# Optimization experiments

Hardware: AMD Instinct MI355X
Metric: run time of the kernel (lower is better)

The kernel has to match this reference:

```python
import jax, jax.numpy as jnp
import numpy as np

B, N, D, H = 4, 1024, 512, 8
DH = D // H  # per-head dim for V and for each of the two Q/K halves
LAM = 0.5


def setup_inputs() -> dict:
    key = jax.random.key(0)
    ks = jax.random.split(key, 7)
    s = 0.02
    return {
        "x": jax.random.normal(ks[0], (B, N, D), dtype=jnp.float32),
        "Wq": jax.random.normal(ks[1], (D, 2 * D), dtype=jnp.float32) * s,
        "bq": jax.random.normal(ks[2], (2 * D,), dtype=jnp.float32) * s,
        "Wk": jax.random.normal(ks[3], (D, 2 * D), dtype=jnp.float32) * s,
        "bk": jax.random.normal(ks[4], (2 * D,), dtype=jnp.float32) * s,
        "Wv": jax.random.normal(ks[5], (D, D), dtype=jnp.float32) * s,
        "bv": jax.random.normal(ks[6], (D,), dtype=jnp.float32) * s,
    }


def reference(x, Wq, bq, Wk, bk, Wv, bv):
    b, n, d = x.shape
    q = (x @ Wq + bq).reshape(b, n, H, 2 * DH).transpose(0, 2, 1, 3)  # [B,H,N,2*DH]
    k = (x @ Wk + bk).reshape(b, n, H, 2 * DH).transpose(0, 2, 1, 3)
    v = (x @ Wv + bv).reshape(b, n, H, DH).transpose(0, 2, 1, 3)      # [B,H,N,DH]
    q1, q2 = q[..., :DH], q[..., DH:]
    k1, k2 = k[..., :DH], k[..., DH:]
    scale = 1.0 / jnp.sqrt(jnp.float32(DH))
    a1 = jax.nn.softmax(jnp.einsum("bhqd,bhkd->bhqk", q1, k1) * scale, axis=-1)
    a2 = jax.nn.softmax(jnp.einsum("bhqd,bhkd->bhqk", q2, k2) * scale, axis=-1)
    attn = a1 - LAM * a2                                              # [B,H,N,N]
    out = jnp.einsum("bhqk,bhkd->bhqd", attn, v)                      # [B,H,N,DH]
    return out.transpose(0, 2, 1, 3).reshape(b, n, d)
```

## Files before the change

### kernel.cpp

```cpp
#include <hip/hip_runtime.h>
#include <hip/hip_bf16.h>

typedef unsigned short u16;
typedef unsigned int u32;
typedef short s16x8 __attribute__((ext_vector_type(8)));
typedef float f32x4 __attribute__((ext_vector_type(4)));

__device__ inline u16 f2bf(float f) {
  union { float f; unsigned int u; } v; v.f = f;
  unsigned int r = v.u + 0x7fffu + ((v.u >> 16) & 1u);
  return (u16)(r >> 16);
}

__device__ __forceinline__ void g2lds16(const u16* g, u16* l) {
  __builtin_amdgcn_global_load_lds((const __attribute__((address_space(1))) void*)g,
                                   (__attribute__((address_space(3))) void*)l, 16, 0, 0);
}

__global__ __launch_bounds__(256) void prep_kernel(const float* __restrict__ x,
                                                   const float* __restrict__ Wq,
                                                   const float* __restrict__ Wk,
                                                   const float* __restrict__ Wv,
                                                   u16* __restrict__ xb, u16* __restrict__ wt) {
  __shared__ float tile[64][65];
  int bid = blockIdx.x;
  if (bid < 1024) {
    int i = (bid * 256 + threadIdx.x) * 8;
    float4 a = *(const float4*)(x + i);
    float4 b = *(const float4*)(x + i + 4);
    s16x8 o;
    o[0] = (short)f2bf(a.x); o[1] = (short)f2bf(a.y);
    o[2] = (short)f2bf(a.z); o[3] = (short)f2bf(a.w);
    o[4] = (short)f2bf(b.x); o[5] = (short)f2bf(b.y);
    o[6] = (short)f2bf(b.z); o[7] = (short)f2bf(b.w);
    *(s16x8*)(xb + i) = o;
    return;
  }
  int t = bid - 1024;
  const float* src; int C, rowoff, j0, k0;
  if (t < 256) {
    src = (t < 128) ? Wq : Wk;
    C = 1024; rowoff = (t < 128) ? 0 : 1024;
    int tt = t & 127;
    j0 = (tt & 15) * 64; k0 = (tt >> 4) * 64;
  } else {
    src = Wv; C = 512; rowoff = 2048;
    int tt = t - 256;
    j0 = (tt & 7) * 64; k0 = (tt >> 3) * 64;
  }
  int tx = threadIdx.x % 64, ty4 = threadIdx.x / 64;
#pragma unroll
  for (int p = 0; p < 16; ++p) {
    int r = p * 4 + ty4;
    tile[r][tx] = src[(size_t)(k0 + r) * C + j0 + tx];
  }
  __syncthreads();
#pragma unroll
  for (int p = 0; p < 16; ++p) {
    int r = p * 4 + ty4;
    wt[(size_t)(rowoff + j0 + r) * 512 + k0 + tx] = f2bf(tile[tx][r]);
  }
}

__global__ __launch_bounds__(256, 3) void gemm_qkv(const u16* __restrict__ xb, const u16* __restrict__ wt,
                                                   const float* __restrict__ bq, const float* __restrict__ bk,
                                                   const float* __restrict__ bv,
                                                   u16* __restrict__ qa, u16* __restrict__ ka,
                                                   u16* __restrict__ va) {
  __shared__ __align__(16) u16 As[128 * 64];
  __shared__ __align__(16) u16 Bs[128 * 64];
  int m0 = blockIdx.x * 128, j0 = blockIdx.y * 128;
  int tid = threadIdx.x;
  int w = tid >> 6, lane = tid & 63, quad = lane >> 4, l16 = lane & 15;
  int wr = (w >> 1) * 64, wc = (w & 1) * 64;

  int srow[4], scol[4], sbase[4];
#pragma unroll
  for (int it = 0; it < 4; ++it) {
    int s = it * 256 + tid;
    srow[it] = s >> 3;
    scol[it] = (s & 7) ^ ((s >> 3) & 7);
    sbase[it] = (s & ~63) * 8;
  }

  f32x4 acc[4][4];
#pragma unroll
  for (int i = 0; i < 4; ++i)
#pragma unroll
    for (int j = 0; j < 4; ++j)
#pragma unroll
      for (int r = 0; r < 4; ++r) acc[i][j][r] = 0.f;

  for (int kk = 0; kk < 8; ++kk) {
    int k0 = kk * 64;
    __syncthreads();
#pragma unroll
    for (int it = 0; it < 4; ++it) {
      g2lds16(xb + (size_t)(m0 + srow[it]) * 512 + k0 + scol[it] * 8, &As[sbase[it]]);
      g2lds16(wt + (size_t)(j0 + srow[it]) * 512 + k0 + scol[it] * 8, &Bs[sbase[it]]);
    }
    __syncthreads();
#pragma unroll
    for (int kb = 0; kb < 2; ++kb) {
      s16x8 af[4], bfr[4];
#pragma unroll
      for (int rb = 0; rb < 4; ++rb) {
        int row = wr + rb * 16 + l16;
        af[rb] = *(const s16x8*)(&As[row * 64 + (((kb * 4 + quad) ^ (row & 7)) * 8)]);
      }
#pragma unroll
      for (int cb = 0; cb < 4; ++cb) {
        int row = wc + cb * 16 + l16;
        bfr[cb] = *(const s16x8*)(&Bs[row * 64 + (((kb * 4 + quad) ^ (row & 7)) * 8)]);
      }
#pragma unroll
      for (int rb = 0; rb < 4; ++rb)
#pragma unroll
        for (int cb = 0; cb < 4; ++cb)
          acc[rb][cb] = __builtin_amdgcn_mfma_f32_16x16x32_bf16(af[rb], bfr[cb], acc[rb][cb], 0, 0, 0);
    }
  }

#pragma unroll
  for (int cb = 0; cb < 4; ++cb) {
    int j = j0 + wc + cb * 16 + l16;
    float bias = (j < 1024) ? bq[j] : (j < 2048) ? bk[j - 1024] : bv[j - 2048];
#pragma unroll
    for (int rb = 0; rb < 4; ++rb) {
#pragma unroll
      for (int r = 0; r < 4; ++r) {
        int m = m0 + wr + rb * 16 + quad * 4 + r;
        int bidx = m >> 10, n = m & 1023;
        u16 o = f2bf(acc[rb][cb][r] + bias);
        if (j < 1024) {
          int h = j >> 7, r2 = j & 127;
          qa[((size_t)((bidx * 8 + h) * 1024 + n)) * 128 + r2] = o;
        } else if (j < 2048) {
          int jj = j - 1024, h = jj >> 7, r2 = jj & 127;
          ka[((size_t)((bidx * 8 + h) * 1024 + n)) * 128 + r2] = o;
        } else {
          int jj = j - 2048, h = jj >> 6, d = jj & 63;
          va[((size_t)((bidx * 8 + h) * 64 + d)) * 1024 + n] = o;
        }
      }
    }
  }
}

__global__ __launch_bounds__(256, 2) void attn_kernel(const u16* __restrict__ qa, const u16* __restrict__ ka,
                                                      const u16* __restrict__ va, float* __restrict__ out) {
  __shared__ __align__(16) u16 smem[12288];
  u16* Ks = smem;
  u16* Vs = smem + 8192;
  float* Ex = (float*)smem;

  int bh = blockIdx.x, b = bh >> 3, h = bh & 7;
  int q0 = blockIdx.y * 32;
  int tid = threadIdx.x, w = tid >> 6, lane = tid & 63, quad = lane >> 4, l16 = lane & 15;
  int kh = w >> 1;
  int qr = q0 + (w & 1) * 16;

  const u16* kgbase = ka + (size_t)bh * 1024 * 128;
  const u16* vgbase = va + (size_t)bh * 64 * 1024;

  const u16* qrow = qa + (size_t)(bh * 1024 + qr + l16) * 128;
  s16x8 qf[2][2];
  qf[0][0] = *(const s16x8*)(qrow + quad * 8);
  qf[0][1] = *(const s16x8*)(qrow + 32 + quad * 8);
  qf[1][0] = *(const s16x8*)(qrow + 64 + quad * 8);
  qf[1][1] = *(const s16x8*)(qrow + 96 + quad * 8);

  f32x4 O1[4], O2[4];
#pragma unroll
  for (int i = 0; i < 4; ++i)
#pragma unroll
    for (int r = 0; r < 4; ++r) { O1[i][r] = 0.f; O2[i][r] = 0.f; }
  float lacc[2] = {0.f, 0.f};

  size_t kgo[4]; int kbse[4];
#pragma unroll
  for (int i = 0; i < 4; ++i) {
    int s = i * 256 + tid;
    int skh = s >> 9, row = (s >> 4) & 31, c = s & 15;
    kgo[i] = (size_t)(skh * 512 + row) * 128 + ((c ^ (row & 7)) * 8);
    kbse[i] = (s & ~63) * 8;
  }
  size_t vgo[2]; int vbse[2];
#pragma unroll
  for (int i = 0; i < 2; ++i) {
    int s = i * 256 + tid;
    int skh = s >> 8, row = (s >> 2) & 63, c = s & 3;
    vgo[i] = (size_t)row * 1024 + skh * 512 + ((c ^ (row & 3)) * 8);
    vbse[i] = (s & ~63) * 8;
  }

  int srcLo = (quad & 1) * 32 + l16;
  int srcHi = srcLo + 16;
  bool hiSel = quad >= 2;

  for (int kt = 0; kt < 16; ++kt) {
    __syncthreads();
#pragma unroll
    for (int i = 0; i < 4; ++i)
      g2lds16(kgbase + kgo[i] + (size_t)kt * 4096, &Ks[kbse[i]]);
#pragma unroll
    for (int i = 0; i < 2; ++i)
      g2lds16(vgbase + vgo[i] + (size_t)kt * 32, &Vs[vbse[i]]);
    __syncthreads();

    s16x8 vf[4];
#pragma unroll
    for (int ct = 0; ct < 4; ++ct) {
      int row = ct * 16 + l16;
      vf[ct] = *(const s16x8*)(&Vs[kh * 2048 + row * 32 + ((quad ^ (row & 3)) * 8)]);
    }

#pragma unroll
    for (int hh = 0; hh < 2; ++hh) {
      u32 pk[2][2];
#pragma unroll
      for (int nt = 0; nt < 2; ++nt) {
        f32x4 sv; sv[0] = sv[1] = sv[2] = sv[3] = 0.f;
#pragma unroll
        for (int kb = 0; kb < 2; ++kb) {
          int row = nt * 16 + l16;
          s16x8 kf = *(const s16x8*)(&Ks[kh * 4096 + row * 128 +
                                         (((hh * 8 + kb * 4 + quad) ^ (row & 7)) * 8)]);
          sv = __builtin_amdgcn_mfma_f32_16x16x32_bf16(kf, qf[hh][kb], sv, 0, 0, 0);
        }
        u32 ue[4];
#pragma unroll
        for (int r = 0; r < 4; ++r) {
          float e = __expf(sv[r] * 0.125f);
          ue[r] = __float_as_uint(e);
          lacc[hh] += __uint_as_float(ue[r] & 0xffff0000u);
        }
        pk[nt][0] = (ue[0] >> 16) | (ue[1] & 0xffff0000u);
        pk[nt][1] = (ue[2] >> 16) | (ue[3] & 0xffff0000u);
      }
      u32 a0 = __shfl(pk[0][0], srcLo), b0 = __shfl(pk[1][0], srcLo);
      u32 a1 = __shfl(pk[0][1], srcLo), b1 = __shfl(pk[1][1], srcLo);
      u32 a2 = __shfl(pk[0][0], srcHi), b2 = __shfl(pk[1][0], srcHi);
      u32 a3 = __shfl(pk[0][1], srcHi), b3 = __shfl(pk[1][1], srcHi);
      union { u32 wv[4]; s16x8 frag; } pu;
      pu.wv[0] = hiSel ? b0 : a0;
      pu.wv[1] = hiSel ? b1 : a1;
      pu.wv[2] = hiSel ? b2 : a2;
      pu.wv[3] = hiSel ? b3 : a3;
      if (hh == 0) {
#pragma unroll
        for (int ct = 0; ct < 4; ++ct)
          O1[ct] = __builtin_amdgcn_mfma_f32_16x16x32_bf16(vf[ct], pu.frag, O1[ct], 0, 0, 0);
      } else {
#pragma unroll
        for (int ct = 0; ct < 4; ++ct)
          O2[ct] = __builtin_amdgcn_mfma_f32_16x16x32_bf16(vf[ct], pu.frag, O2[ct], 0, 0, 0);
      }
    }
  }
  __syncthreads();

  if (w >= 2) {
    int base = ((w - 2) * 64 + lane) * 35;
#pragma unroll
    for (int ct = 0; ct < 4; ++ct)
#pragma unroll
      for (int r = 0; r < 4; ++r) {
        Ex[base + ct * 4 + r] = O1[ct][r];
        Ex[base + 16 + ct * 4 + r] = O2[ct][r];
      }
    Ex[base + 32] = lacc[0];
    Ex[base + 33] = lacc[1];
  }
  __syncthreads();
  if (w < 2) {
    int base = (w * 64 + lane) * 35;
#pragma unroll
    for (int ct = 0; ct < 4; ++ct)
#pragma unroll
      for (int r = 0; r < 4; ++r) {
        O1[ct][r] += Ex[base + ct * 4 + r];
        O2[ct][r] += Ex[base + 16 + ct * 4 + r];
      }
    float l1 = lacc[0] + Ex[base + 32];
    float l2 = lacc[1] + Ex[base + 33];
    l1 += __shfl_xor(l1, 16); l1 += __shfl_xor(l1, 32);
    l2 += __shfl_xor(l2, 16); l2 += __shfl_xor(l2, 32);
    float inv1 = 1.0f / l1, inv2 = 1.0f / l2;
    float* orow = out + (size_t)(b * 1024 + qr + l16) * 512 + h * 64;
#pragma unroll
    for (int ct = 0; ct < 4; ++ct) {
      float4 v;
      v.x = O1[ct][0] * inv1 - 0.5f * O2[ct][0] * inv2;
      v.y = O1[ct][1] * inv1 - 0.5f * O2[ct][1] * inv2;
      v.z = O1[ct][2] * inv1 - 0.5f * O2[ct][2] * inv2;
      v.w = O1[ct][3] * inv1 - 0.5f * O2[ct][3] * inv2;
      *(float4*)(orow + ct * 16 + quad * 4) = v;
    }
  }
}

extern "C" void kernel_launch(void* const* d_in, const int* in_sizes, int n_in,
                              void* d_out, int out_size, void* d_ws, size_t ws_size,
                              hipStream_t stream) {
  (void)in_sizes; (void)n_in; (void)out_size; (void)ws_size;
  const float* x  = (const float*)d_in[0];
  const float* Wq = (const float*)d_in[1];
  const float* bq = (const float*)d_in[2];
  const float* Wk = (const float*)d_in[3];
  const float* bk = (const float*)d_in[4];
  const float* Wv = (const float*)d_in[5];
  const float* bv = (const float*)d_in[6];
  float* out = (float*)d_out;

  char* ws = (char*)d_ws;
  u16* xb = (u16*)(ws);
  u16* wt = (u16*)(ws + 4194304);
  u16* qa = (u16*)(ws + 6815744);
  u16* ka = (u16*)(ws + 15204352);
  u16* va = (u16*)(ws + 23592960);

  prep_kernel<<<1344, 256, 0, stream>>>(x, Wq, Wk, Wv, xb, wt);
  gemm_qkv<<<dim3(32, 20), 256, 0, stream>>>(xb, wt, bq, bk, bv, qa, ka, va);
  attn_kernel<<<dim3(32, 32), 256, 0, stream>>>(qa, ka, va, out);
}
```

Measured before the change: 139.4 us.

## Load K/V fragments directly from global memory instead of staging through LDS

The attention kernel no longer stages K and V tiles into shared memory with global_load_lds and barrier pairs. Each wave now reads its MFMA K and V fragments straight from global memory, relying on L1/L2 for reuse across waves. Shared memory shrinks to the final reduction buffer, the per-tile __syncthreads pairs are removed, and launch bounds rise to three blocks per CU with the key loop unrolled by two. The cost is redundant global traffic, since the two waves sharing a key half each load the same K/V data. It also risks higher per-load latency and register pressure under the tighter occupancy bound.

```diff
diff --git a/kernel.cpp b/kernel.cpp
--- a/kernel.cpp
+++ b/kernel.cpp
@@ -147,21 +147,17 @@
   }
 }
 
-__global__ __launch_bounds__(256, 2) void attn_kernel(const u16* __restrict__ qa, const u16* __restrict__ ka,
+__global__ __launch_bounds__(256, 3) void attn_kernel(const u16* __restrict__ qa, const u16* __restrict__ ka,
                                                       const u16* __restrict__ va, float* __restrict__ out) {
-  __shared__ __align__(16) u16 smem[12288];
-  u16* Ks = smem;
-  u16* Vs = smem + 8192;
-  float* Ex = (float*)smem;
-
+  __shared__ float Ex[2 * 64 * 35];
   int bh = blockIdx.x, b = bh >> 3, h = bh & 7;
   int q0 = blockIdx.y * 32;
   int tid = threadIdx.x, w = tid >> 6, lane = tid & 63, quad = lane >> 4, l16 = lane & 15;
   int kh = w >> 1;
   int qr = q0 + (w & 1) * 16;
 
-  const u16* kgbase = ka + (size_t)bh * 1024 * 128;
-  const u16* vgbase = va + (size_t)bh * 64 * 1024;
+  const u16* kb0 = ka + (size_t)bh * 1024 * 128 + (size_t)kh * 512 * 128;
+  const u16* vb0 = va + (size_t)bh * 64 * 1024 + kh * 512;
 
   const u16* qrow = qa + (size_t)(bh * 1024 + qr + l16) * 128;
   s16x8 qf[2][2];
@@ -177,43 +173,19 @@
     for (int r = 0; r < 4; ++r) { O1[i][r] = 0.f; O2[i][r] = 0.f; }
   float lacc[2] = {0.f, 0.f};
 
-  size_t kgo[4]; int kbse[4];
-#pragma unroll
-  for (int i = 0; i < 4; ++i) {
-    int s = i * 256 + tid;
-    int skh = s >> 9, row = (s >> 4) & 31, c = s & 15;
-    kgo[i] = (size_t)(skh * 512 + row) * 128 + ((c ^ (row & 7)) * 8);
-    kbse[i] = (s & ~63) * 8;
-  }
-  size_t vgo[2]; int vbse[2];
-#pragma unroll
-  for (int i = 0; i < 2; ++i) {
-    int s = i * 256 + tid;
-    int skh = s >> 8, row = (s >> 2) & 63, c = s & 3;
-    vgo[i] = (size_t)row * 1024 + skh * 512 + ((c ^ (row & 3)) * 8);
-    vbse[i] = (s & ~63) * 8;
-  }
-
   int srcLo = (quad & 1) * 32 + l16;
   int srcHi = srcLo + 16;
   bool hiSel = quad >= 2;
 
+#pragma unroll 2
   for (int kt = 0; kt < 16; ++kt) {
-    __syncthreads();
-#pragma unroll
-    for (int i = 0; i < 4; ++i)
-      g2lds16(kgbase + kgo[i] + (size_t)kt * 4096, &Ks[kbse[i]]);
-#pragma unroll
-    for (int i = 0; i < 2; ++i)
-      g2lds16(vgbase + vgo[i] + (size_t)kt * 32, &Vs[vbse[i]]);
-    __syncthreads();
+    const u16* ktk = kb0 + kt * 32 * 128;
+    const u16* ktv = vb0 + kt * 32;
 
     s16x8 vf[4];
 #pragma unroll
-    for (int ct = 0; ct < 4; ++ct) {
-      int row = ct * 16 + l16;
-      vf[ct] = *(const s16x8*)(&Vs[kh * 2048 + row * 32 + ((quad ^ (row & 3)) * 8)]);
-    }
+    for (int ct = 0; ct < 4; ++ct)
+      vf[ct] = *(const s16x8*)(ktv + (size_t)(ct * 16 + l16) * 1024 + quad * 8);
 
 #pragma unroll
     for (int hh = 0; hh < 2; ++hh) {
@@ -222,11 +194,9 @@
       for (int nt = 0; nt < 2; ++nt) {
         f32x4 sv; sv[0] = sv[1] = sv[2] = sv[3] = 0.f;
 #pragma unroll
-        for (int kb = 0; kb < 2; ++kb) {
-          int row = nt * 16 + l16;
-          s16x8 kf = *(const s16x8*)(&Ks[kh * 4096 + row * 128 +
-                                         (((hh * 8 + kb * 4 + quad) ^ (row & 7)) * 8)]);
-          sv = __builtin_amdgcn_mfma_f32_16x16x32_bf16(kf, qf[hh][kb], sv, 0, 0, 0);
+        for (int kbi = 0; kbi < 2; ++kbi) {
+          s16x8 kf = *(const s16x8*)(ktk + (size_t)(nt * 16 + l16) * 128 + hh * 64 + kbi * 32 + quad * 8);
+          sv = __builtin_amdgcn_mfma_f32_16x16x32_bf16(kf, qf[hh][kbi], sv, 0, 0, 0);
         }
         u32 ue[4];
 #pragma unroll
@@ -258,7 +228,6 @@
       }
     }
   }
-  __syncthreads();
 
   if (w >= 2) {
     int base = ((w - 2) * 64 + lane) * 35;
```

New measurement: 186.4 us. 1.34x slower.
